# Kernel tuning notes

Measured on AMD Instinct MI355X. Metric: run time of the kernel, lower is better.

Reference implementation:

```python
import jax, jax.numpy as jnp
import numpy as np


def setup_inputs() -> dict:
    key = jax.random.key(0)
    kq, ks, kr, kx, ky = jax.random.split(key, 5)
    B, C, H, W, K = 2, 64, 128, 256, 32
    Q = jax.random.normal(kq, (B, C, H, W), dtype=jnp.float32)
    S = jax.random.normal(ks, (B, C, H, W), dtype=jnp.float32)
    R = jax.random.normal(kr, (B, C, H, W), dtype=jnp.float32)
    Pos_x = jax.random.randint(kx, (H * W, K), 0, H, dtype=jnp.int64 if jax.config.jax_enable_x64 else jnp.int32)
    Pos_y = jax.random.randint(ky, (H * W, K), 0, W, dtype=jnp.int64 if jax.config.jax_enable_x64 else jnp.int32)
    return {"Q": Q, "S": S, "R": R, "Pos_x": Pos_x, "Pos_y": Pos_y}


def reference(Q, S, R, Pos_x, Pos_y):
    B, C, H, W = Q.shape
    N = H * W
    px = Pos_x.reshape(-1)  # [N*K]
    py = Pos_y.reshape(-1)
    K = px.shape[0] // N
    # Gather keys/values at candidate positions: [B, C, N*K] -> [B, C, N, K]
    Key = S[:, :, px, py].reshape(B, C, N, K)
    Value = R[:, :, px, py].reshape(B, C, N, K)
    # Queries: [B, N, C]
    Qf = Q.reshape(B, C, N).transpose(0, 2, 1)
    # Per-pixel scores over K candidates (NO 1/sqrt(d) scaling, as in original)
    score = jnp.einsum('bnc,bcnk->bnk', Qf, Key)
    attn = jax.nn.softmax(score, axis=-1)
    # Attention-weighted sum of values: [B, N, C]
    out = jnp.einsum('bnk,bcnk->bnc', attn, Value)
    return out.reshape(B, H, W, C).transpose(0, 3, 1, 2)
```

## Files before the change

kernel.cpp:

```cpp
#include <hip/hip_runtime.h>
#include <hip/hip_fp16.h>

constexpr int B = 2, C = 64, H = 128, W = 256, N = H * W, K = 32;

typedef _Float16 hf2 __attribute__((ext_vector_type(2)));

template <int CTRL>
__device__ __forceinline__ float dppf(float x) {
    int i = __builtin_bit_cast(int, x);
    int r = __builtin_amdgcn_update_dpp(i, i, CTRL, 0xF, 0xF, false);
    return __builtin_bit_cast(float, r);
}

__device__ __forceinline__ unsigned sel4(const uint4& v, int g) {
    return g == 0 ? v.x : g == 1 ? v.y : g == 2 ? v.z : v.w;
}
__device__ __forceinline__ unsigned sel4(const ushort4& v, int g) {
    return g == 0 ? v.x : g == 1 ? v.y : g == 2 ? v.z : v.w;
}

__global__ __launch_bounds__(256) void fepam_prep(
    const float* __restrict__ Q, const float* __restrict__ S,
    const float* __restrict__ R,
    const int* __restrict__ Px, const int* __restrict__ Py,
    __half* __restrict__ Qt, __half* __restrict__ St, __half* __restrict__ Rt,
    unsigned short* __restrict__ Idx) {
    const int n0 = blockIdx.x * 64;
    const int b  = blockIdx.y;
    const int z  = blockIdx.z;

    if (z == 3) {
        if (b) return;
#pragma unroll
        for (int t = 0; t < 8; ++t) {
            const int e  = threadIdx.x + 256 * t;
            const int nl = e >> 5, k = e & 31;
            const int n  = n0 + nl;
            const int idx = Px[(size_t)n * K + k] * W + Py[(size_t)n * K + k];
            Idx[(size_t)n * K + (k & 7) * 4 + (k >> 3)] = (unsigned short)idx;
        }
        return;
    }

    __shared__ float tile[C][65];
    const float* src = (z == 0 ? S : (z == 1 ? R : Q)) + (size_t)b * C * N;
    __half2* d2 = (__half2*)((z == 0 ? St : (z == 1 ? Rt : Qt)) +
                             (size_t)b * N * C);
    {
        const int j = threadIdx.x & 63, c0 = threadIdx.x >> 6;
        const float* s = src + n0 + j;
#pragma unroll
        for (int r = 0; r < 16; ++r) {
            int c = c0 + r * 4;
            tile[c][j] = s[(size_t)c * N];
        }
    }
    __syncthreads();
    {
        const int c2 = threadIdx.x & 31, j0 = threadIdx.x >> 5;
#pragma unroll
        for (int r = 0; r < 8; ++r) {
            int j = j0 + 8 * r;
            d2[(size_t)(n0 + j) * 32 + c2] =
                __floats2half2_rn(tile[2 * c2][j], tile[2 * c2 + 1][j]);
        }
    }
}

__global__ __launch_bounds__(256, 6) void fepam_scores(
    const __half* __restrict__ Qt, const unsigned short* __restrict__ Idx,
    const __half* __restrict__ St, unsigned* __restrict__ AI) {
    const int tid  = threadIdx.x;
    const int lane = tid & 63;
    const int wave = tid >> 6;
    const int bx   = blockIdx.x;
    const int b    = bx & 1;
    const int n0   = (bx >> 1) * 32 + wave * 8;

    const int c_oct = lane & 7;
    const int k_loc = lane >> 3;

    const __half* Qtb = Qt + (size_t)b * N * C;
    const __half* Stb = St + (size_t)b * N * C;
    unsigned* AIb = AI + (size_t)b * N * K;

    auto ldi = [&](int p) {
        return *(const ushort4*)(Idx + (size_t)(n0 + p) * K + k_loc * 4);
    };
    auto ldq = [&](int p) {
        return *(const float4*)(Qtb + (size_t)(n0 + p) * C + c_oct * 8);
    };
    auto ldk = [&](const ushort4& iv, int g) {
        return *(const float4*)(Stb + ((size_t)sel4(iv, g) << 6) + c_oct * 8);
    };

    ushort4 iv_c = ldi(0), iv_n = ldi(1);
    float4  q_c  = ldq(0), q_n  = ldq(1);
    float4  k_c[4];
#pragma unroll
    for (int g = 0; g < 4; ++g) k_c[g] = ldk(iv_c, g);

#pragma unroll
    for (int p = 0; p < 8; ++p) {
        float4 k_n[4];
        if (p < 7) {
#pragma unroll
            for (int g = 0; g < 4; ++g) k_n[g] = ldk(iv_n, g);
        }
        ushort4 iv_2;
        float4  q_2;
        if (p < 6) { iv_2 = ldi(p + 2); q_2 = ldq(p + 2); }

        float s[4];
#pragma unroll
        for (int g = 0; g < 4; ++g) {
            const hf2* k2 = (const hf2*)&k_c[g];
            const hf2* q2 = (const hf2*)&q_c;
            float acc = 0.f;
#pragma unroll
            for (int u = 0; u < 4; ++u)
                acc = __builtin_amdgcn_fdot2(k2[u], q2[u], acc, false);
            s[g] = acc;
        }
#pragma unroll
        for (int g = 0; g < 4; ++g) {
            s[g] += dppf<0xB1>(s[g]);
            s[g] += dppf<0x4E>(s[g]);
            s[g] += dppf<0x141>(s[g]);
        }
        float m = fmaxf(fmaxf(s[0], s[1]), fmaxf(s[2], s[3]));
        m = fmaxf(m, dppf<0x128>(m));
        m = fmaxf(m, __shfl_xor(m, 16));
        m = fmaxf(m, __shfl_xor(m, 32));
        float e0 = __expf(s[0] - m), e1 = __expf(s[1] - m);
        float e2 = __expf(s[2] - m), e3 = __expf(s[3] - m);
        float l = (e0 + e1) + (e2 + e3);
        l += dppf<0x128>(l);
        l += __shfl_xor(l, 16);
        l += __shfl_xor(l, 32);
        const float inv = 1.0f / l;

        if (c_oct == 0) {
            uint4 wv;
            wv.x = ((unsigned)iv_c.x << 16) |
                   __half_as_ushort(__float2half_rn(e0 * inv));
            wv.y = ((unsigned)iv_c.y << 16) |
                   __half_as_ushort(__float2half_rn(e1 * inv));
            wv.z = ((unsigned)iv_c.z << 16) |
                   __half_as_ushort(__float2half_rn(e2 * inv));
            wv.w = ((unsigned)iv_c.w << 16) |
                   __half_as_ushort(__float2half_rn(e3 * inv));
            *(uint4*)(AIb + (size_t)(n0 + p) * K + k_loc * 4) = wv;
        }

#pragma unroll
        for (int g = 0; g < 4; ++g) k_c[g] = k_n[g];
        iv_c = iv_n; q_c = q_n;
        iv_n = iv_2; q_n = q_2;
    }
}

__global__ __launch_bounds__(256, 6) void fepam_values(
    const unsigned* __restrict__ AI, const __half* __restrict__ Rt,
    float* __restrict__ Out) {
    __shared__ __align__(16) float ot[32][66];

    const int tid  = threadIdx.x;
    const int lane = tid & 63;
    const int wave = tid >> 6;
    const int bx   = blockIdx.x;
    const int b    = bx & 1;
    const int n0t  = (bx >> 1) * 32;
    const int n0   = n0t + wave * 8;

    const int c_oct = lane & 7;
    const int k_loc = lane >> 3;
    const bool hi8  = (lane & 8)  != 0;
    const bool hi16 = (lane & 16) != 0;
    const bool hi32 = (lane & 32) != 0;

    const __half* Rtb = Rt + (size_t)b * N * C;
    const unsigned* AIb = AI + (size_t)b * N * K;

    auto ldw = [&](int p) {
        return *(const uint4*)(AIb + (size_t)(n0 + p) * K + k_loc * 4);
    };
    auto ldv = [&](const uint4& wv, int g) {
        return *(const float4*)(Rtb + ((size_t)(sel4(wv, g) >> 16) << 6) +
                                c_oct * 8);
    };

    uint4  w_c = ldw(0), w_n = ldw(1);
    float4 v_c[4];
#pragma unroll
    for (int g = 0; g < 4; ++g) v_c[g] = ldv(w_c, g);

#pragma unroll
    for (int p = 0; p < 8; ++p) {
        float4 v_n[4];
        if (p < 7) {
#pragma unroll
            for (int g = 0; g < 4; ++g) v_n[g] = ldv(w_n, g);
        }
        uint4 w_2;
        if (p < 6) w_2 = ldw(p + 2);

        const float a[4] = {
            __half2float(__ushort_as_half((unsigned short)(w_c.x & 0xffffu))),
            __half2float(__ushort_as_half((unsigned short)(w_c.y & 0xffffu))),
            __half2float(__ushort_as_half((unsigned short)(w_c.z & 0xffffu))),
            __half2float(__ushort_as_half((unsigned short)(w_c.w & 0xffffu)))};
        float acc[8] = {0, 0, 0, 0, 0, 0, 0, 0};
#pragma unroll
        for (int g = 0; g < 4; ++g) {
            const __half2* v2 = (const __half2*)&v_c[g];
#pragma unroll
            for (int u = 0; u < 4; ++u) {
                const float2 vf = __half22float2(v2[u]);
                acc[2 * u]     = fmaf(a[g], vf.x, acc[2 * u]);
                acc[2 * u + 1] = fmaf(a[g], vf.y, acc[2 * u + 1]);
            }
        }

        float r4[4];
#pragma unroll
        for (int i = 0; i < 4; ++i) {
            const float send = hi8 ? acc[i] : acc[4 + i];
            const float recv = dppf<0x128>(send);
            r4[i] = (hi8 ? acc[4 + i] : acc[i]) + recv;
        }
        float r2[2];
#pragma unroll
        for (int i = 0; i < 2; ++i) {
            const float send = hi16 ? r4[i] : r4[2 + i];
            const float recv = __shfl_xor(send, 16);
            r2[i] = (hi16 ? r4[2 + i] : r4[i]) + recv;
        }
        {
            const float send = hi32 ? r2[0] : r2[1];
            const float recv = __shfl_xor(send, 32);
            const float r1   = (hi32 ? r2[1] : r2[0]) + recv;
            const int c = c_oct * 8 + (hi8 ? 4 : 0) + (hi16 ? 2 : 0) + (hi32 ? 1 : 0);
            ot[wave * 8 + p][c] = r1;
        }

#pragma unroll
        for (int g = 0; g < 4; ++g) v_c[g] = v_n[g];
        w_c = w_n;
        w_n = w_2;
    }
    __syncthreads();

    {
        const int j = tid & 31, c0 = tid >> 5;
        float* od = Out + (size_t)b * C * N + n0t + j;
#pragma unroll
        for (int r = 0; r < 8; ++r) {
            int c = c0 + r * 8;
            od[(size_t)c * N] = ot[j][c];
        }
    }
}

extern "C" void kernel_launch(void* const* d_in, const int* in_sizes, int n_in,
                              void* d_out, int out_size, void* d_ws, size_t ws_size,
                              hipStream_t stream) {
    const float* Q  = (const float*)d_in[0];
    const float* S  = (const float*)d_in[1];
    const float* R  = (const float*)d_in[2];
    const int*   Px = (const int*)d_in[3];
    const int*   Py = (const int*)d_in[4];
    float* Out = (float*)d_out;

    __half* St = (__half*)d_ws;
    __half* Rt = St + (size_t)B * N * C;
    __half* Qt = Rt + (size_t)B * N * C;
    unsigned short* Idx = (unsigned short*)(Qt + (size_t)B * N * C);
    unsigned* AI = (unsigned*)(Idx + (size_t)N * K);

    dim3 pgrid(N / 64, B, 4);
    fepam_prep<<<pgrid, 256, 0, stream>>>(Q, S, R, Px, Py, Qt, St, Rt, Idx);

    dim3 ggrid(N / 32 * B);
    fepam_scores<<<ggrid, 256, 0, stream>>>(Qt, Idx, St, AI);
    fepam_values<<<ggrid, 256, 0, stream>>>(AI, Rt, Out);
}
```

Before: 137.2 us.

## Deepen gather prefetch to two pixels per stage and spread index prep over batch blocks

The scores and values kernels now work on pairs of pixels. Each stage prefetches the gathered key or value rows for the next two pixels, plus indices and queries two pairs ahead, so more random-gather loads are in flight per wave. Launch-bound occupancy drops from 6 to 4 to make room for the extra registers. The index-packing path in the prep kernel now splits its work across both batch-index blocks instead of leaving one idle. The cost is higher register pressure and fewer resident waves to hide latency.

```diff
diff --git a/kernel.cpp b/kernel.cpp
--- a/kernel.cpp
+++ b/kernel.cpp
@@ -30,10 +30,9 @@
     const int z  = blockIdx.z;
 
     if (z == 3) {
-        if (b) return;
-#pragma unroll
-        for (int t = 0; t < 8; ++t) {
-            const int e  = threadIdx.x + 256 * t;
+#pragma unroll
+        for (int t = 0; t < 4; ++t) {
+            const int e  = b * 1024 + threadIdx.x + 256 * t;
             const int nl = e >> 5, k = e & 31;
             const int n  = n0 + nl;
             const int idx = Px[(size_t)n * K + k] * W + Py[(size_t)n * K + k];
@@ -67,7 +66,7 @@
     }
 }
 
-__global__ __launch_bounds__(256, 6) void fepam_scores(
+__global__ __launch_bounds__(256, 4) void fepam_scores(
     const __half* __restrict__ Qt, const unsigned short* __restrict__ Idx,
     const __half* __restrict__ St, unsigned* __restrict__ AI) {
     const int tid  = threadIdx.x;
@@ -94,73 +93,90 @@
         return *(const float4*)(Stb + ((size_t)sel4(iv, g) << 6) + c_oct * 8);
     };
 
-    ushort4 iv_c = ldi(0), iv_n = ldi(1);
-    float4  q_c  = ldq(0), q_n  = ldq(1);
-    float4  k_c[4];
-#pragma unroll
-    for (int g = 0; g < 4; ++g) k_c[g] = ldk(iv_c, g);
-
-#pragma unroll
-    for (int p = 0; p < 8; ++p) {
-        float4 k_n[4];
-        if (p < 7) {
-#pragma unroll
-            for (int g = 0; g < 4; ++g) k_n[g] = ldk(iv_n, g);
-        }
-        ushort4 iv_2;
-        float4  q_2;
-        if (p < 6) { iv_2 = ldi(p + 2); q_2 = ldq(p + 2); }
-
-        float s[4];
-#pragma unroll
-        for (int g = 0; g < 4; ++g) {
-            const hf2* k2 = (const hf2*)&k_c[g];
-            const hf2* q2 = (const hf2*)&q_c;
-            float acc = 0.f;
-#pragma unroll
-            for (int u = 0; u < 4; ++u)
-                acc = __builtin_amdgcn_fdot2(k2[u], q2[u], acc, false);
-            s[g] = acc;
-        }
-#pragma unroll
-        for (int g = 0; g < 4; ++g) {
-            s[g] += dppf<0xB1>(s[g]);
-            s[g] += dppf<0x4E>(s[g]);
-            s[g] += dppf<0x141>(s[g]);
-        }
-        float m = fmaxf(fmaxf(s[0], s[1]), fmaxf(s[2], s[3]));
-        m = fmaxf(m, dppf<0x128>(m));
-        m = fmaxf(m, __shfl_xor(m, 16));
-        m = fmaxf(m, __shfl_xor(m, 32));
-        float e0 = __expf(s[0] - m), e1 = __expf(s[1] - m);
-        float e2 = __expf(s[2] - m), e3 = __expf(s[3] - m);
-        float l = (e0 + e1) + (e2 + e3);
-        l += dppf<0x128>(l);
-        l += __shfl_xor(l, 16);
-        l += __shfl_xor(l, 32);
-        const float inv = 1.0f / l;
-
-        if (c_oct == 0) {
-            uint4 wv;
-            wv.x = ((unsigned)iv_c.x << 16) |
-                   __half_as_ushort(__float2half_rn(e0 * inv));
-            wv.y = ((unsigned)iv_c.y << 16) |
-                   __half_as_ushort(__float2half_rn(e1 * inv));
-            wv.z = ((unsigned)iv_c.z << 16) |
-                   __half_as_ushort(__float2half_rn(e2 * inv));
-            wv.w = ((unsigned)iv_c.w << 16) |
-                   __half_as_ushort(__float2half_rn(e3 * inv));
-            *(uint4*)(AIb + (size_t)(n0 + p) * K + k_loc * 4) = wv;
-        }
-
-#pragma unroll
-        for (int g = 0; g < 4; ++g) k_c[g] = k_n[g];
-        iv_c = iv_n; q_c = q_n;
-        iv_n = iv_2; q_n = q_2;
-    }
-}
-
-__global__ __launch_bounds__(256, 6) void fepam_values(
+    ushort4 ivA[2] = {ldi(0), ldi(1)};
+    ushort4 ivB[2] = {ldi(2), ldi(3)};
+    float4  qA[2]  = {ldq(0), ldq(1)};
+    float4  qB[2]  = {ldq(2), ldq(3)};
+    float4  kA[2][4];
+#pragma unroll
+    for (int pp = 0; pp < 2; ++pp)
+#pragma unroll
+        for (int g = 0; g < 4; ++g) kA[pp][g] = ldk(ivA[pp], g);
+
+#pragma unroll
+    for (int pair = 0; pair < 4; ++pair) {
+        const int pbase = pair * 2;
+
+        float4 kB[2][4];
+        if (pair < 3) {
+#pragma unroll
+            for (int pp = 0; pp < 2; ++pp)
+#pragma unroll
+                for (int g = 0; g < 4; ++g) kB[pp][g] = ldk(ivB[pp], g);
+        }
+        ushort4 ivC[2];
+        float4  qC[2];
+        if (pair < 2) {
+            ivC[0] = ldi(pbase + 4); ivC[1] = ldi(pbase + 5);
+            qC[0]  = ldq(pbase + 4); qC[1]  = ldq(pbase + 5);
+        }
+
+#pragma unroll
+        for (int pp = 0; pp < 2; ++pp) {
+            float s[4];
+#pragma unroll
+            for (int g = 0; g < 4; ++g) {
+                const hf2* k2 = (const hf2*)&kA[pp][g];
+                const hf2* q2 = (const hf2*)&qA[pp];
+                float acc = 0.f;
+#pragma unroll
+                for (int u = 0; u < 4; ++u)
+                    acc = __builtin_amdgcn_fdot2(k2[u], q2[u], acc, false);
+                s[g] = acc;
+            }
+#pragma unroll
+            for (int g = 0; g < 4; ++g) {
+                s[g] += dppf<0xB1>(s[g]);
+                s[g] += dppf<0x4E>(s[g]);
+                s[g] += dppf<0x141>(s[g]);
+            }
+            float m = fmaxf(fmaxf(s[0], s[1]), fmaxf(s[2], s[3]));
+            m = fmaxf(m, dppf<0x128>(m));
+            m = fmaxf(m, __shfl_xor(m, 16));
+            m = fmaxf(m, __shfl_xor(m, 32));
+            float e0 = __expf(s[0] - m), e1 = __expf(s[1] - m);
+            float e2 = __expf(s[2] - m), e3 = __expf(s[3] - m);
+            float l = (e0 + e1) + (e2 + e3);
+            l += dppf<0x128>(l);
+            l += __shfl_xor(l, 16);
+            l += __shfl_xor(l, 32);
+            const float inv = 1.0f / l;
+
+            if (c_oct == 0) {
+                uint4 wv;
+                wv.x = ((unsigned)ivA[pp].x << 16) |
+                       __half_as_ushort(__float2half_rn(e0 * inv));
+                wv.y = ((unsigned)ivA[pp].y << 16) |
+                       __half_as_ushort(__float2half_rn(e1 * inv));
+                wv.z = ((unsigned)ivA[pp].z << 16) |
+                       __half_as_ushort(__float2half_rn(e2 * inv));
+                wv.w = ((unsigned)ivA[pp].w << 16) |
+                       __half_as_ushort(__float2half_rn(e3 * inv));
+                *(uint4*)(AIb + (size_t)(n0 + pbase + pp) * K + k_loc * 4) = wv;
+            }
+        }
+
+#pragma unroll
+        for (int pp = 0; pp < 2; ++pp) {
+#pragma unroll
+            for (int g = 0; g < 4; ++g) kA[pp][g] = kB[pp][g];
+            ivA[pp] = ivB[pp]; qA[pp] = qB[pp];
+            ivB[pp] = ivC[pp]; qB[pp] = qC[pp];
+        }
+    }
+}
+
+__global__ __launch_bounds__(256, 4) void fepam_values(
     const unsigned* __restrict__ AI, const __half* __restrict__ Rt,
     float* __restrict__ Out) {
     __shared__ __align__(16) float ot[32][66];
@@ -190,64 +206,79 @@
                                 c_oct * 8);
     };
 
-    uint4  w_c = ldw(0), w_n = ldw(1);
-    float4 v_c[4];
-#pragma unroll
-    for (int g = 0; g < 4; ++g) v_c[g] = ldv(w_c, g);
-
-#pragma unroll
-    for (int p = 0; p < 8; ++p) {
-        float4 v_n[4];
-        if (p < 7) {
-#pragma unroll
-            for (int g = 0; g < 4; ++g) v_n[g] = ldv(w_n, g);
-        }
-        uint4 w_2;
-        if (p < 6) w_2 = ldw(p + 2);
-
-        const float a[4] = {
-            __half2float(__ushort_as_half((unsigned short)(w_c.x & 0xffffu))),
-            __half2float(__ushort_as_half((unsigned short)(w_c.y & 0xffffu))),
-            __half2float(__ushort_as_half((unsigned short)(w_c.z & 0xffffu))),
-            __half2float(__ushort_as_half((unsigned short)(w_c.w & 0xffffu)))};
-        float acc[8] = {0, 0, 0, 0, 0, 0, 0, 0};
-#pragma unroll
-        for (int g = 0; g < 4; ++g) {
-            const __half2* v2 = (const __half2*)&v_c[g];
-#pragma unroll
-            for (int u = 0; u < 4; ++u) {
-                const float2 vf = __half22float2(v2[u]);
-                acc[2 * u]     = fmaf(a[g], vf.x, acc[2 * u]);
-                acc[2 * u + 1] = fmaf(a[g], vf.y, acc[2 * u + 1]);
-            }
-        }
-
-        float r4[4];
-#pragma unroll
-        for (int i = 0; i < 4; ++i) {
-            const float send = hi8 ? acc[i] : acc[4 + i];
-            const float recv = dppf<0x128>(send);
-            r4[i] = (hi8 ? acc[4 + i] : acc[i]) + recv;
-        }
-        float r2[2];
-#pragma unroll
-        for (int i = 0; i < 2; ++i) {
-            const float send = hi16 ? r4[i] : r4[2 + i];
-            const float recv = __shfl_xor(send, 16);
-            r2[i] = (hi16 ? r4[2 + i] : r4[i]) + recv;
-        }
-        {
-            const float send = hi32 ? r2[0] : r2[1];
-            const float recv = __shfl_xor(send, 32);
-            const float r1   = (hi32 ? r2[1] : r2[0]) + recv;
-            const int c = c_oct * 8 + (hi8 ? 4 : 0) + (hi16 ? 2 : 0) + (hi32 ? 1 : 0);
-            ot[wave * 8 + p][c] = r1;
-        }
-
-#pragma unroll
-        for (int g = 0; g < 4; ++g) v_c[g] = v_n[g];
-        w_c = w_n;
-        w_n = w_2;
+    uint4 wA[2] = {ldw(0), ldw(1)};
+    uint4 wB[2] = {ldw(2), ldw(3)};
+    float4 vA[2][4];
+#pragma unroll
+    for (int pp = 0; pp < 2; ++pp)
+#pragma unroll
+        for (int g = 0; g < 4; ++g) vA[pp][g] = ldv(wA[pp], g);
+
+#pragma unroll
+    for (int pair = 0; pair < 4; ++pair) {
+        const int pbase = pair * 2;
+
+        float4 vB[2][4];
+        if (pair < 3) {
+#pragma unroll
+            for (int pp = 0; pp < 2; ++pp)
+#pragma unroll
+                for (int g = 0; g < 4; ++g) vB[pp][g] = ldv(wB[pp], g);
+        }
+        uint4 wC[2];
+        if (pair < 2) { wC[0] = ldw(pbase + 4); wC[1] = ldw(pbase + 5); }
+
+#pragma unroll
+        for (int pp = 0; pp < 2; ++pp) {
+            const uint4 wc = wA[pp];
+            const float a[4] = {
+                __half2float(__ushort_as_half((unsigned short)(wc.x & 0xffffu))),
+                __half2float(__ushort_as_half((unsigned short)(wc.y & 0xffffu))),
+                __half2float(__ushort_as_half((unsigned short)(wc.z & 0xffffu))),
+                __half2float(__ushort_as_half((unsigned short)(wc.w & 0xffffu)))};
+            float acc[8] = {0, 0, 0, 0, 0, 0, 0, 0};
+#pragma unroll
+            for (int g = 0; g < 4; ++g) {
+                const __half2* v2 = (const __half2*)&vA[pp][g];
+#pragma unroll
+                for (int u = 0; u < 4; ++u) {
+                    const float2 vf = __half22float2(v2[u]);
+                    acc[2 * u]     = fmaf(a[g], vf.x, acc[2 * u]);
+                    acc[2 * u + 1] = fmaf(a[g], vf.y, acc[2 * u + 1]);
+                }
+            }
+
+            float r4[4];
+#pragma unroll
+            for (int i = 0; i < 4; ++i) {
+                const float send = hi8 ? acc[i] : acc[4 + i];
+                const float recv = dppf<0x128>(send);
+                r4[i] = (hi8 ? acc[4 + i] : acc[i]) + recv;
+            }
+            float r2[2];
+#pragma unroll
+            for (int i = 0; i < 2; ++i) {
+                const float send = hi16 ? r4[i] : r4[2 + i];
+                const float recv = __shfl_xor(send, 16);
+                r2[i] = (hi16 ? r4[2 + i] : r4[i]) + recv;
+            }
+            {
+                const float send = hi32 ? r2[0] : r2[1];
+                const float recv = __shfl_xor(send, 32);
+                const float r1   = (hi32 ? r2[1] : r2[0]) + recv;
+                const int c = c_oct * 8 + (hi8 ? 4 : 0) + (hi16 ? 2 : 0) +
+                              (hi32 ? 1 : 0);
+                ot[wave * 8 + pbase + pp][c] = r1;
+            }
+        }
+
+#pragma unroll
+        for (int pp = 0; pp < 2; ++pp) {
+#pragma unroll
+            for (int g = 0; g < 4; ++g) vA[pp][g] = vB[pp][g];
+            wA[pp] = wB[pp];
+            wB[pp] = wC[pp];
+        }
     }
     __syncthreads();
 
```

Measured after the change: 139.4 us. Within noise of the previous version (+1.6%).
